# Optimization experiments

Measured on AMD Instinct MI355X. Metric: run time of the kernel, lower is better.

Reference implementation:

```python
import jax, jax.numpy as jnp
import numpy as np

B, T, D, H = 4, 2048, 1024, 16
DH = D // H  # 64

def setup_inputs() -> dict:
    key = jax.random.key(0)
    ks = jax.random.split(key, 5)
    scale = 1.0 / np.sqrt(DH)
    return {
        "x": jax.random.normal(ks[0], (B, T, D), dtype=jnp.float32),
        "Wq": jax.random.normal(ks[1], (H, DH, DH), dtype=jnp.float32) * scale,
        "Wk": jax.random.normal(ks[2], (H, DH, DH), dtype=jnp.float32) * scale,
        "Wv": jax.random.normal(ks[3], (H, DH, DH), dtype=jnp.float32) * scale,
        "Wout": jax.random.normal(ks[4], (D, D), dtype=jnp.float32) * (1.0 / np.sqrt(D)),
    }

def reference(x, Wq, Wk, Wv, Wout):
    b, t, d = x.shape
    xh = x.reshape(b, t, H, DH)  # split into heads (b, t, h, dh)
    # torch Linear: y = x @ W.T -> contract input dim with last dim of W
    Q = jnp.einsum('bthd,hed->bthe', xh, Wq)
    K = jnp.einsum('bthd,hed->bthe', xh, Wk)
    V = jnp.einsum('bthd,hed->bthe', xh, Wv)
    scale = 1.0 / jnp.sqrt(jnp.asarray(DH, dtype=x.dtype))
    scores = jnp.einsum('bqhd,bkhd->bhqk', Q, K) * scale  # (b, h, T, T)
    weights = jax.nn.softmax(scores, axis=-1)
    attn = jnp.einsum('bhqk,bkhd->bqhd', weights, V)  # (b, T, h, dh)
    attn = attn.reshape(b, t, d)  # concat heads
    return attn @ Wout.T
```

## Files before the change

kernel.cpp:

```cpp
#include <hip/hip_runtime.h>
#include <hip/hip_bf16.h>

#define BB 4
#define TT 2048
#define DD 1024
#define HH 16

typedef __bf16 bf16;
typedef __bf16 bf16x8 __attribute__((ext_vector_type(8)));
typedef __bf16 bf16x4 __attribute__((ext_vector_type(4)));
typedef float f32x4 __attribute__((ext_vector_type(4)));
typedef float f32x16 __attribute__((ext_vector_type(16)));
typedef unsigned int u32;
typedef u32 u32x4 __attribute__((ext_vector_type(4)));

#define MFMA16(a, b, c) __builtin_amdgcn_mfma_f32_16x16x32_bf16(a, b, c, 0, 0, 0)
#define MFMA32(a, b, c) __builtin_amdgcn_mfma_f32_32x32x16_bf16(a, b, c, 0, 0, 0)

#define C1 0.18033688011112042f

typedef __attribute__((address_space(1))) const u32 gau32;
typedef __attribute__((address_space(3))) u32 lau32;
static __device__ __forceinline__ void gload_lds16(const void* g, void* l) {
    __builtin_amdgcn_global_load_lds((gau32*)g, (lau32*)l, 16, 0, 0);
}

static __device__ __forceinline__ u32 cvtpk(float a, float b) {
    u32 r;
    asm("v_cvt_pk_bf16_f32 %0, %1, %2" : "=v"(r) : "v"(a), "v"(b));
    return r;
}

static __device__ __forceinline__ float rexp2(float x) {
#if __has_builtin(__builtin_amdgcn_exp2f)
    return __builtin_amdgcn_exp2f(x);
#else
    float r;
    asm("v_exp_f32 %0, %1" : "=v"(r) : "v"(x));
    return r;
#endif
}

__global__ __launch_bounds__(256) void k_cvtall(const float* __restrict__ wo, const float* __restrict__ wq,
                                                const float* __restrict__ wk, const float* __restrict__ wv,
                                                bf16* __restrict__ ob, bf16* __restrict__ qb,
                                                bf16* __restrict__ kb, bf16* __restrict__ vb) {
    int i = (blockIdx.x * 256 + threadIdx.x) * 4;
    const float* s;
    bf16* d;
    int off;
    if (i < DD * DD) {
        s = wo; d = ob; off = i;
    } else {
        int j = i - DD * DD;
        int wsel = j >> 16;
        off = j & 65535;
        s = wsel == 0 ? wq : (wsel == 1 ? wk : wv);
        d = wsel == 0 ? qb : (wsel == 1 ? kb : vb);
    }
    f32x4 v = *reinterpret_cast<const f32x4*>(s + off);
    bf16x4 r;
    r[0] = (bf16)v[0]; r[1] = (bf16)v[1]; r[2] = (bf16)v[2]; r[3] = (bf16)v[3];
    *reinterpret_cast<bf16x4*>(d + off) = r;
}

__global__ __launch_bounds__(256) void k_qkv(const float* __restrict__ x,
                                             const bf16* __restrict__ Wq,
                                             const bf16* __restrict__ Wk,
                                             const bf16* __restrict__ Wv,
                                             bf16* __restrict__ Qb,
                                             bf16* __restrict__ Kb,
                                             bf16* __restrict__ VT) {
    __shared__ float xs[4][32 * 64];
    const int w = threadIdx.x >> 6, lane = threadIdx.x & 63;
    const int c = lane & 15, g = lane >> 4;
    const int bh = blockIdx.y;
    const int b = bh >> 4, h = bh & 15;
    const int tb = blockIdx.x * 128 + w * 32;

    float* xw = xs[w];
    {
        const int lr = lane >> 4;
        const int lch = lane & 15;
#pragma unroll
        for (int p = 0; p < 8; p++) {
            const int r = p * 4 + lr;
            const int ch = lch ^ (r & 15);
            gload_lds16(x + ((size_t)(b * TT + tb + r)) * DD + h * 64 + ch * 4,
                        (char*)xw + p * 1024);
        }
    }
    asm volatile("s_waitcnt vmcnt(0)" ::: "memory");

    bf16x8 a[2][2];
#pragma unroll
    for (int s = 0; s < 2; s++)
#pragma unroll
        for (int dt = 0; dt < 2; dt++) {
            const int r = 16 * s + c;
            const int c0 = 8 * dt + 2 * g;
            f32x4 lo = *reinterpret_cast<const f32x4*>(&xw[r * 64 + (c0 ^ (r & 15)) * 4]);
            f32x4 hi = *reinterpret_cast<const f32x4*>(&xw[r * 64 + ((c0 + 1) ^ (r & 15)) * 4]);
            u32x4 u;
            u[0] = cvtpk(lo[0], lo[1]);
            u[1] = cvtpk(lo[2], lo[3]);
            u[2] = cvtpk(hi[0], hi[1]);
            u[3] = cvtpk(hi[2], hi[3]);
            a[s][dt] = __builtin_bit_cast(bf16x8, u);
        }

    const bf16* const Ws[3] = {Wq, Wk, Wv};
    f32x4 acc[3][2][4];
#pragma unroll
    for (int m = 0; m < 3; m++)
#pragma unroll
        for (int s = 0; s < 2; s++)
#pragma unroll
            for (int e = 0; e < 4; e++)
#pragma unroll
                for (int r = 0; r < 4; r++) acc[m][s][e][r] = 0.0f;

#pragma unroll
    for (int m = 0; m < 3; m++) {
#pragma unroll
        for (int eg = 0; eg < 4; eg++) {
#pragma unroll
            for (int dt = 0; dt < 2; dt++) {
                bf16x8 bf = *reinterpret_cast<const bf16x8*>(
                    Ws[m] + (size_t)(h * 64 + 16 * eg + c) * 64 + 32 * dt + 8 * g);
#pragma unroll
                for (int s = 0; s < 2; s++)
                    acc[m][s][eg] = MFMA16(a[s][dt], bf, acc[m][s][eg]);
            }
        }
    }

    bf16* const outs[2] = {Qb, Kb};
#pragma unroll
    for (int m = 0; m < 2; m++)
#pragma unroll
        for (int s = 0; s < 2; s++)
#pragma unroll
            for (int eg = 0; eg < 4; eg++)
#pragma unroll
                for (int r = 0; r < 4; r++) {
                    int t = tb + 16 * s + 4 * g + r;
                    float sv = acc[m][s][eg][r];
                    if (m == 0) sv *= C1;
                    outs[m][((size_t)bh * TT + t) * 64 + 16 * eg + c] = (bf16)sv;
                }

    bf16* vl = (bf16*)xs[w];
#pragma unroll
    for (int s = 0; s < 2; s++)
#pragma unroll
        for (int eg = 0; eg < 4; eg++) {
            bf16x4 v4;
#pragma unroll
            for (int r = 0; r < 4; r++) v4[r] = (bf16)acc[2][s][eg][r];
            *reinterpret_cast<bf16x4*>(&vl[(16 * eg + c) * 40 + 16 * s + 4 * g]) = v4;
        }
#pragma unroll
    for (int n = 0; n < 8; n++) {
        const int np = (n & 4) | ((n & 1) << 1) | ((n >> 1) & 1);
        bf16x4 v = *reinterpret_cast<bf16x4*>(&vl[lane * 40 + 4 * n]);
        *reinterpret_cast<bf16x4*>(&VT[((size_t)bh * 64 + lane) * TT + tb + 4 * np]) = v;
    }
}

#define ATTN_STEP(SKC, SVC, SKP, SVP, T, ISSUE, VM)                                             \
    do {                                                                                        \
        asm volatile("s_waitcnt vmcnt(" VM ")" ::: "memory");                                   \
        __builtin_amdgcn_s_barrier();                                                           \
        __builtin_amdgcn_sched_barrier(0);                                                      \
        if (ISSUE) {                                                                            \
            gload_lds16(kgsrc + (size_t)((T) + 2) * 4096, &(SKP)[w * 512]);                     \
            gload_lds16(vgsrc + (size_t)((T) + 2) * 64, &(SVP)[w * 512]);                       \
        }                                                                                       \
        f32x16 s0, s1;                                                                          \
        _Pragma("unroll") for (int i = 0; i < 16; i++) { s0[i] = 0.0f; s1[i] = 0.0f; }          \
        __builtin_amdgcn_s_setprio(1);                                                          \
        _Pragma("unroll") for (int d = 0; d < 4; d++) {                                         \
            bf16x8 ka0 = *reinterpret_cast<const bf16x8*>(&(SKC)[roff + d * 1024 + goff0]);     \
            bf16x8 ka1 = *reinterpret_cast<const bf16x8*>(&(SKC)[roff + d * 1024 + goff1]);     \
            s0 = MFMA32(ka0, aq[d], s0);                                                        \
            s1 = MFMA32(ka1, aq[d], s1);                                                        \
        }                                                                                       \
        __builtin_amdgcn_s_setprio(0);                                                          \
        u32 pk[2][4][2];                                                                        \
        _Pragma("unroll") for (int r = 0; r < 16; r++) { float p = rexp2(s0[r]); psum += p; s0[r] = p; } \
        _Pragma("unroll") for (int r = 0; r < 16; r++) { float p = rexp2(s1[r]); psum += p; s1[r] = p; } \
        _Pragma("unroll") for (int m = 0; m < 4; m++)                                           \
            _Pragma("unroll") for (int b2 = 0; b2 < 2; b2++) {                                  \
                pk[0][m][b2] = cvtpk(s0[4 * m + 2 * b2], s0[4 * m + 2 * b2 + 1]);               \
                pk[1][m][b2] = cvtpk(s1[4 * m + 2 * b2], s1[4 * m + 2 * b2 + 1]);               \
            }                                                                                   \
        __builtin_amdgcn_s_setprio(1);                                                          \
        _Pragma("unroll") for (int kt = 0; kt < 4; kt++) {                                      \
            u32x4 pu;                                                                           \
            pu[0] = pk[kt >> 1][2 * (kt & 1)][0];                                               \
            pu[1] = pk[kt >> 1][2 * (kt & 1)][1];                                               \
            pu[2] = pk[kt >> 1][2 * (kt & 1) + 1][0];                                           \
            pu[3] = pk[kt >> 1][2 * (kt & 1) + 1][1];                                           \
            bf16x8 pb = __builtin_bit_cast(bf16x8, pu);                                         \
            bf16x8 va0 = *reinterpret_cast<const bf16x8*>(&(SVC)[roff + kt * 1024 + goff0]);    \
            bf16x8 va1 = *reinterpret_cast<const bf16x8*>(&(SVC)[roff + kt * 1024 + goff1]);    \
            o0 = MFMA32(va0, pb, o0);                                                           \
            o1 = MFMA32(va1, pb, o1);                                                           \
        }                                                                                       \
        __builtin_amdgcn_s_setprio(0);                                                         \
    } while (0)

__global__ __launch_bounds__(512, 4) void k_attn(const bf16* __restrict__ Qb,
                                                 const bf16* __restrict__ Kb,
                                                 const bf16* __restrict__ VT,
                                                 bf16* __restrict__ AO) {
    __shared__ bf16 sK[3][64 * 64];
    __shared__ bf16 sV[3][64 * 64];
    const int w = threadIdx.x >> 6, lane = threadIdx.x & 63;
    const int q = lane & 31, h = lane >> 5;
    const int bid = blockIdx.x;
    const int swz = (bid & 7) * 64 + (bid >> 3);
    const int bh = swz >> 3;
    const int qb = (swz & 7) * 256 + w * 32;
    const bf16* Qh = Qb + (size_t)bh * TT * 64;
    const bf16* Kh = Kb + (size_t)bh * TT * 64;
    const bf16* Vh = VT + (size_t)bh * 64 * TT;

    const int gp = lane & 7;
    const int rp = w * 8 + (lane >> 3);
    const int u_ = rp & 15, J1 = rp >> 4;
    const int e_ = gp ^ (u_ & 7);
    const int st = 32 * (e_ >> 2) + 16 * (e_ & 1) + u_;
    const int sj = 2 * J1 + ((e_ >> 1) & 1);
    const bf16* kgsrc = Kh + (size_t)st * 64 + sj * 8;
    const bf16* vgsrc = Vh + (size_t)st * TT + sj * 8;

    gload_lds16(kgsrc, &sK[0][w * 512]);
    gload_lds16(vgsrc, &sV[0][w * 512]);
    gload_lds16(kgsrc + 4096, &sK[1][w * 512]);
    gload_lds16(vgsrc + 64, &sV[1][w * 512]);

    bf16x8 aq[4];
#pragma unroll
    for (int d = 0; d < 4; d++)
        aq[d] = *reinterpret_cast<const bf16x8*>(Qh + (size_t)(qb + q) * 64 + 16 * d + 8 * h);

    const int vv = 2 * h + ((q >> 4) & 1);
    const int gl = vv ^ (q & 3);
    const int gb2 = (q >> 2) & 1;
    const int roff = (q & 15) * 64;
    const int goff0 = (4 * gb2 + gl) * 8;
    const int goff1 = (4 * (1 ^ gb2) + gl) * 8;

    f32x16 o0, o1;
#pragma unroll
    for (int i = 0; i < 16; i++) { o0[i] = 0.0f; o1[i] = 0.0f; }
    float psum = 0.0f;

#pragma unroll 1
    for (int i = 0; i < 10; i++) {
        const int t0 = 3 * i;
        ATTN_STEP(sK[0], sV[0], sK[2], sV[2], t0, 1, "2");
        ATTN_STEP(sK[1], sV[1], sK[0], sV[0], t0 + 1, 1, "2");
        ATTN_STEP(sK[2], sV[2], sK[1], sV[1], t0 + 2, 1, "2");
    }
    ATTN_STEP(sK[0], sV[0], sK[2], sV[2], 30, 0, "2");
    ATTN_STEP(sK[1], sV[1], sK[0], sV[0], 31, 0, "0");

    const float l = psum + __shfl_xor(psum, 32);
    const float linv = 1.0f / l;

    const size_t obase = ((size_t)bh * TT + qb + q) * 64;
#pragma unroll
    for (int dg = 0; dg < 2; dg++)
#pragma unroll
        for (int m = 0; m < 4; m++) {
            bf16x4 v;
#pragma unroll
            for (int j = 0; j < 4; j++) {
                const float ov = dg ? o1[4 * m + j] : o0[4 * m + j];
                v[j] = (bf16)(ov * linv);
            }
            *reinterpret_cast<bf16x4*>(AO + obase + 32 * dg + 8 * m + 4 * h) = v;
        }
}

#define OSTAGE(BUF, H)                                                                          \
    do {                                                                                        \
        const bf16* Ab = AO + ((size_t)(b * HH + (H)) * TT + t0) * 64;                          \
        const bf16* Bb = Wo + (size_t)nb * DD + (H) * 64;                                       \
        _Pragma("unroll") for (int p = 0; p < 4; p++) {                                         \
            const int r = p * 32 + w * 8 + (lane >> 3);                                         \
            const int jj = (lane & 7) ^ (r & 7);                                                \
            gload_lds16(Ab + (size_t)r * 64 + jj * 8, &sA[BUF][p * 2048 + w * 512]);            \
            gload_lds16(Bb + (size_t)r * DD + jj * 8, &sB[BUF][p * 2048 + w * 512]);            \
        }                                                                                       \
    } while (0)

__global__ __launch_bounds__(256, 2) void k_oproj(const bf16* __restrict__ AO,
                                                  const bf16* __restrict__ Wo,
                                                  float* __restrict__ out) {
    __shared__ bf16 sA[2][128 * 64];
    __shared__ bf16 sB[2][128 * 64];
    const int w = threadIdx.x >> 6, lane = threadIdx.x & 63;
    const int c = lane & 15, g = lane >> 4;
    const int bid = blockIdx.x;
    const int nb = (bid & 7) * 128;
    const int row0 = (bid >> 3) * 128;
    const int b = row0 >> 11;
    const int t0 = row0 & 2047;

    f32x4 acc[2][8];
#pragma unroll
    for (int s = 0; s < 2; s++)
#pragma unroll
        for (int ng = 0; ng < 8; ng++)
#pragma unroll
            for (int r = 0; r < 4; r++) acc[s][ng][r] = 0.0f;

    OSTAGE(0, 0);
    __syncthreads();

    int buf = 0;
#pragma unroll 1
    for (int hh = 0; hh < 16; hh++) {
        if (hh < 15) OSTAGE(buf ^ 1, hh + 1);
        const bf16* pa = sA[buf];
        const bf16* pb = sB[buf];
#pragma unroll
        for (int dt = 0; dt < 2; dt++) {
            const int gsw = ((4 * dt + g) ^ (c & 7)) * 8;
            bf16x8 aa[2];
#pragma unroll
            for (int s = 0; s < 2; s++)
                aa[s] = *reinterpret_cast<const bf16x8*>(&pa[(w * 32 + 16 * s + c) * 64 + gsw]);
            __builtin_amdgcn_s_setprio(1);
#pragma unroll
            for (int ng = 0; ng < 8; ng++) {
                bf16x8 bb = *reinterpret_cast<const bf16x8*>(&pb[(16 * ng + c) * 64 + gsw]);
#pragma unroll
                for (int s = 0; s < 2; s++)
                    acc[s][ng] = MFMA16(aa[s], bb, acc[s][ng]);
            }
            __builtin_amdgcn_s_setprio(0);
        }
        __syncthreads();
        buf ^= 1;
    }

    const int mb = row0 + w * 32;
#pragma unroll
    for (int s = 0; s < 2; s++)
#pragma unroll
        for (int ng = 0; ng < 8; ng++)
#pragma unroll
            for (int r = 0; r < 4; r++)
                out[(size_t)(mb + 16 * s + 4 * g + r) * DD + nb + 16 * ng + c] = acc[s][ng][r];
}

extern "C" void kernel_launch(void* const* d_in, const int* in_sizes, int n_in,
                              void* d_out, int out_size, void* d_ws, size_t ws_size,
                              hipStream_t stream) {
    const float* x = (const float*)d_in[0];
    const float* Wq = (const float*)d_in[1];
    const float* Wk = (const float*)d_in[2];
    const float* Wv = (const float*)d_in[3];
    const float* Wo = (const float*)d_in[4];
    float* out = (float*)d_out;

    char* ws = (char*)d_ws;
    bf16* Qb = (bf16*)(ws);
    bf16* Kb = (bf16*)(ws + (16ll << 20));
    bf16* VT = (bf16*)(ws + (32ll << 20));
    bf16* AO = (bf16*)(ws + (48ll << 20));
    bf16* Wob = (bf16*)(ws + (64ll << 20));
    bf16* Wqb = (bf16*)(ws + (66ll << 20));
    bf16* Wkb = (bf16*)(ws + (66ll << 20) + (128ll << 10));
    bf16* Wvb = (bf16*)(ws + (66ll << 20) + (256ll << 10));

    k_cvtall<<<1216, 256, 0, stream>>>(Wo, Wq, Wk, Wv, Wob, Wqb, Wkb, Wvb);
    k_qkv<<<dim3(TT / 128, BB * HH), 256, 0, stream>>>(x, Wqb, Wkb, Wvb, Qb, Kb, VT);
    k_attn<<<512, 512, 0, stream>>>(Qb, Kb, VT, AO);
    k_oproj<<<512, 256, 0, stream>>>(AO, Wob, out);
}
```

Measured before the change: 134.0 us.

## Triple-buffer the output-projection GEMM with half-size K tiles and explicit vmcnt waits

The output-projection kernel now uses K tiles of 32 instead of 64 and rotates through three LDS buffers instead of two. Loads run two stages ahead, and each step uses one vmcnt wait plus one barrier in place of the trailing __syncthreads. This is meant to hide global-to-LDS latency and cut barrier stalls between tiles. The XOR swizzle on the LDS layout is dropped, which may add bank conflicts on the bf16x8 LDS reads, and each step does less MFMA work per barrier.

```diff
diff --git a/kernel.cpp b/kernel.cpp
--- a/kernel.cpp
+++ b/kernel.cpp
@@ -286,23 +286,44 @@
         }
 }
 
-#define OSTAGE(BUF, H)                                                                          \
+#define OSTAGE(BUF, KK)                                                                         \
     do {                                                                                        \
-        const bf16* Ab = AO + ((size_t)(b * HH + (H)) * TT + t0) * 64;                          \
-        const bf16* Bb = Wo + (size_t)nb * DD + (H) * 64;                                       \
-        _Pragma("unroll") for (int p = 0; p < 4; p++) {                                         \
-            const int r = p * 32 + w * 8 + (lane >> 3);                                         \
-            const int jj = (lane & 7) ^ (r & 7);                                                \
-            gload_lds16(Ab + (size_t)r * 64 + jj * 8, &sA[BUF][p * 2048 + w * 512]);            \
-            gload_lds16(Bb + (size_t)r * DD + jj * 8, &sB[BUF][p * 2048 + w * 512]);            \
-        }                                                                                       \
+        const int h_ = (KK) >> 1, dc_ = ((KK) & 1) * 32;                                        \
+        const bf16* Ab = AO + ((size_t)(b * HH + h_) * TT + t0) * 64 + dc_;                     \
+        const bf16* Bb = Wo + (size_t)nb * DD + (KK) * 32;                                      \
+        _Pragma("unroll") for (int p = 0; p < 2; p++) {                                         \
+            const int r = (w * 2 + p) * 16 + (lane >> 2);                                       \
+            const int ch = lane & 3;                                                            \
+            gload_lds16(Ab + (size_t)r * 64 + ch * 8, &(sA[BUF])[(w * 2 + p) * 512]);           \
+            gload_lds16(Bb + (size_t)r * DD + ch * 8, &(sB[BUF])[(w * 2 + p) * 512]);           \
+        }                                                                                       \
+    } while (0)
+
+#define OSTEP(BUF, PBUF, KK, ISSUE, VM)                                                         \
+    do {                                                                                        \
+        asm volatile("s_waitcnt vmcnt(" VM ")" ::: "memory");                                   \
+        __builtin_amdgcn_s_barrier();                                                           \
+        __builtin_amdgcn_sched_barrier(0);                                                      \
+        if (ISSUE) OSTAGE(PBUF, (KK) + 2);                                                      \
+        const bf16* pa = sA[BUF];                                                               \
+        const bf16* pb = sB[BUF];                                                               \
+        bf16x8 aa[2];                                                                           \
+        _Pragma("unroll") for (int s = 0; s < 2; s++)                                           \
+            aa[s] = *reinterpret_cast<const bf16x8*>(&pa[(w * 32 + 16 * s + c) * 32 + 8 * g]);  \
+        __builtin_amdgcn_s_setprio(1);                                                          \
+        _Pragma("unroll") for (int ng = 0; ng < 8; ng++) {                                      \
+            bf16x8 bb = *reinterpret_cast<const bf16x8*>(&pb[(16 * ng + c) * 32 + 8 * g]);      \
+            _Pragma("unroll") for (int s = 0; s < 2; s++)                                       \
+                acc[s][ng] = MFMA16(aa[s], bb, acc[s][ng]);                                     \
+        }                                                                                       \
+        __builtin_amdgcn_s_setprio(0);                                                          \
     } while (0)
 
 __global__ __launch_bounds__(256, 2) void k_oproj(const bf16* __restrict__ AO,
                                                   const bf16* __restrict__ Wo,
                                                   float* __restrict__ out) {
-    __shared__ bf16 sA[2][128 * 64];
-    __shared__ bf16 sB[2][128 * 64];
+    __shared__ bf16 sA[3][128 * 32];
+    __shared__ bf16 sB[3][128 * 32];
     const int w = threadIdx.x >> 6, lane = threadIdx.x & 63;
     const int c = lane & 15, g = lane >> 4;
     const int bid = blockIdx.x;
@@ -320,34 +341,17 @@
             for (int r = 0; r < 4; r++) acc[s][ng][r] = 0.0f;
 
     OSTAGE(0, 0);
-    __syncthreads();
-
-    int buf = 0;
+    OSTAGE(1, 1);
+
 #pragma unroll 1
-    for (int hh = 0; hh < 16; hh++) {
-        if (hh < 15) OSTAGE(buf ^ 1, hh + 1);
-        const bf16* pa = sA[buf];
-        const bf16* pb = sB[buf];
-#pragma unroll
-        for (int dt = 0; dt < 2; dt++) {
-            const int gsw = ((4 * dt + g) ^ (c & 7)) * 8;
-            bf16x8 aa[2];
-#pragma unroll
-            for (int s = 0; s < 2; s++)
-                aa[s] = *reinterpret_cast<const bf16x8*>(&pa[(w * 32 + 16 * s + c) * 64 + gsw]);
-            __builtin_amdgcn_s_setprio(1);
-#pragma unroll
-            for (int ng = 0; ng < 8; ng++) {
-                bf16x8 bb = *reinterpret_cast<const bf16x8*>(&pb[(16 * ng + c) * 64 + gsw]);
-#pragma unroll
-                for (int s = 0; s < 2; s++)
-                    acc[s][ng] = MFMA16(aa[s], bb, acc[s][ng]);
-            }
-            __builtin_amdgcn_s_setprio(0);
-        }
-        __syncthreads();
-        buf ^= 1;
-    }
+    for (int i = 0; i < 10; i++) {
+        const int k0 = 3 * i;
+        OSTEP(0, 2, k0, 1, "4");
+        OSTEP(1, 0, k0 + 1, 1, "4");
+        OSTEP(2, 1, k0 + 2, 1, "4");
+    }
+    OSTEP(0, 2, 30, 0, "4");
+    OSTEP(1, 0, 31, 0, "0");
 
     const int mb = row0 + w * 32;
 #pragma unroll
```

Measured after the change: 137.8 us. +2.8%, slower.

## Switch attention K/V pipeline to double-buffered 128-key tiles

Applied to the files above, without the earlier changes.

Changes the attention main loop from a triple-buffered pipeline of 64-key tiles (one barrier per tile) to a double-buffered pipeline of 128-key tiles processed as two 64-key halves. The goal is to halve the number of barriers and waitcnt stalls per key sweep. LDS use grows from 6 to 8 tiles of 64x64 bf16, and the wait is now vmcnt(0) with only one tile in flight, so load latency may be hidden less well. Higher LDS use may also reduce occupancy.

```diff
diff --git a/kernel.cpp b/kernel.cpp
--- a/kernel.cpp
+++ b/kernel.cpp
@@ -168,15 +168,8 @@
     }
 }
 
-#define ATTN_STEP(SKC, SVC, SKP, SVP, T, ISSUE, VM)                                             \
+#define ATTN_HALF(SKC, SVC)                                                                     \
     do {                                                                                        \
-        asm volatile("s_waitcnt vmcnt(" VM ")" ::: "memory");                                   \
-        __builtin_amdgcn_s_barrier();                                                           \
-        __builtin_amdgcn_sched_barrier(0);                                                      \
-        if (ISSUE) {                                                                            \
-            gload_lds16(kgsrc + (size_t)((T) + 2) * 4096, &(SKP)[w * 512]);                     \
-            gload_lds16(vgsrc + (size_t)((T) + 2) * 64, &(SVP)[w * 512]);                       \
-        }                                                                                       \
         f32x16 s0, s1;                                                                          \
         _Pragma("unroll") for (int i = 0; i < 16; i++) { s0[i] = 0.0f; s1[i] = 0.0f; }          \
         __builtin_amdgcn_s_setprio(1);                                                          \
@@ -208,15 +201,15 @@
             o0 = MFMA32(va0, pb, o0);                                                           \
             o1 = MFMA32(va1, pb, o1);                                                           \
         }                                                                                       \
-        __builtin_amdgcn_s_setprio(0);                                                         \
+        __builtin_amdgcn_s_setprio(0);                                                          \
     } while (0)
 
 __global__ __launch_bounds__(512, 4) void k_attn(const bf16* __restrict__ Qb,
                                                  const bf16* __restrict__ Kb,
                                                  const bf16* __restrict__ VT,
                                                  bf16* __restrict__ AO) {
-    __shared__ bf16 sK[3][64 * 64];
-    __shared__ bf16 sV[3][64 * 64];
+    __shared__ bf16 sK[2][128 * 64];
+    __shared__ bf16 sV[2][128 * 64];
     const int w = threadIdx.x >> 6, lane = threadIdx.x & 63;
     const int q = lane & 31, h = lane >> 5;
     const int bid = blockIdx.x;
@@ -237,9 +230,9 @@
     const bf16* vgsrc = Vh + (size_t)st * TT + sj * 8;
 
     gload_lds16(kgsrc, &sK[0][w * 512]);
+    gload_lds16(kgsrc + 4096, &sK[0][4096 + w * 512]);
     gload_lds16(vgsrc, &sV[0][w * 512]);
-    gload_lds16(kgsrc + 4096, &sK[1][w * 512]);
-    gload_lds16(vgsrc + 64, &sV[1][w * 512]);
+    gload_lds16(vgsrc + 64, &sV[0][4096 + w * 512]);
 
     bf16x8 aq[4];
 #pragma unroll
@@ -259,14 +252,22 @@
     float psum = 0.0f;
 
 #pragma unroll 1
-    for (int i = 0; i < 10; i++) {
-        const int t0 = 3 * i;
-        ATTN_STEP(sK[0], sV[0], sK[2], sV[2], t0, 1, "2");
-        ATTN_STEP(sK[1], sV[1], sK[0], sV[0], t0 + 1, 1, "2");
-        ATTN_STEP(sK[2], sV[2], sK[1], sV[1], t0 + 2, 1, "2");
-    }
-    ATTN_STEP(sK[0], sV[0], sK[2], sV[2], 30, 0, "2");
-    ATTN_STEP(sK[1], sV[1], sK[0], sV[0], 31, 0, "0");
+    for (int t = 0; t < 16; t++) {
+        asm volatile("s_waitcnt vmcnt(0)" ::: "memory");
+        __builtin_amdgcn_s_barrier();
+        __builtin_amdgcn_sched_barrier(0);
+        const int buf = t & 1;
+        if (t < 15) {
+            gload_lds16(kgsrc + (size_t)(t + 1) * 8192, &sK[buf ^ 1][w * 512]);
+            gload_lds16(kgsrc + (size_t)(t + 1) * 8192 + 4096, &sK[buf ^ 1][4096 + w * 512]);
+            gload_lds16(vgsrc + (size_t)(t + 1) * 128, &sV[buf ^ 1][w * 512]);
+            gload_lds16(vgsrc + (size_t)(t + 1) * 128 + 64, &sV[buf ^ 1][4096 + w * 512]);
+        }
+        const bf16* sk = &sK[buf][0];
+        const bf16* sv = &sV[buf][0];
+        ATTN_HALF(sk, sv);
+        ATTN_HALF((sk + 4096), (sv + 4096));
+    }
 
     const float l = psum + __shfl_xor(psum, 32);
     const float linv = 1.0f / l;
```

Result: slower. 137.0 us (+2.2%).
